# Performance work log

Measured on AMD Instinct MI355X. Metric: run time of the kernel, lower is better.

## Reference

```python
import jax, jax.numpy as jnp
import numpy as np
import math

B, I, O, SEG = 128, 2048, 2048, 10

def setup_inputs() -> dict:
    key = jax.random.key(0)
    k1, k2, k3, k4 = jax.random.split(key, 4)
    scale = 1.0 / math.sqrt(I)
    return {
        "x": jax.random.normal(k1, (B, I), dtype=jnp.float32),
        "context": jax.random.normal(k2, (O,), dtype=jnp.float32),
        "prev_activation": jax.random.normal(k3, (B, O), dtype=jnp.float32),
        "weight": jax.random.normal(k4, (O, I), dtype=jnp.float32) * scale,
        "bias": jnp.zeros((O,), dtype=jnp.float32),
        "astrocyte_activation": jnp.ones((O,), dtype=jnp.float32),
        "dendrite_segments": jax.random.normal(jax.random.fold_in(key, 7), (O, I, SEG), dtype=jnp.float32) * scale,
    }

def reference(x, context, prev_activation, weight, bias, astrocyte_activation, dendrite_segments):
    # Astrocyte gating of the linear weight: sigmoid(astro * context) -> [o]
    astro_mod = jax.nn.sigmoid(astrocyte_activation * context)
    # Dendritic branch: relu(einsum('bi,oij->boj')) summed over segments -> [b, o]
    dendritic_out = jnp.maximum(jnp.einsum('bi,oij->boj', x, dendrite_segments), 0.0).sum(axis=2)
    # Gated linear: F.linear(x, weight * astro_mod[:, None], bias) -> [b, o]
    out = x @ (weight * astro_mod[:, None]).T + bias
    # Note: torch's STDP/Hebbian weight mutations (synaptic_tag, protein_synthesis,
    # homeostatic scaling) occur AFTER 'out' is computed and do not affect the
    # returned tensor; they are pure parameter side effects, so omitted here.
    return out + dendritic_out
```

## Files before the change

### kernel.cpp

```cpp
#include <hip/hip_runtime.h>
#include <hip/hip_bf16.h>

#define B_ 128
#define I_ 2048
#define O_ 2048
#define SEG 10
#define BK 32
#define NST (I_ / BK)
#define XTILE 8192
#define DCH 1280
#define DLS 1408

typedef __attribute__((ext_vector_type(8))) short bf16x8;
typedef __attribute__((ext_vector_type(4))) float f32x4;

static __device__ __forceinline__ unsigned short f2bf(float f) {
    unsigned u = __float_as_uint(f);
    u += 0x7FFFu + ((u >> 16) & 1u);
    return (unsigned short)(u >> 16);
}

static __device__ __forceinline__ unsigned cvt2(float lo, float hi) {
    __hip_bfloat162 h = __float22bfloat162_rn(make_float2(lo, hi));
    return *reinterpret_cast<unsigned*>(&h);
}

#define GLDS16(SRC, DST) \
    __builtin_amdgcn_global_load_lds( \
        (const __attribute__((address_space(1))) unsigned*)(SRC), \
        (__attribute__((address_space(3))) unsigned*)(DST), 16, 0, 0)
#define GLDS4(SRC, DST) \
    __builtin_amdgcn_global_load_lds( \
        (const __attribute__((address_space(1))) unsigned*)(SRC), \
        (__attribute__((address_space(3))) unsigned*)(DST), 4, 0, 0)

#define WAITVM(N) asm volatile("s_waitcnt vmcnt(" #N ")" ::: "memory")
#define BARRIER() do { __builtin_amdgcn_sched_barrier(0); \
                       __builtin_amdgcn_s_barrier(); \
                       __builtin_amdgcn_sched_barrier(0); } while (0)

__global__ void xconv(const float* __restrict__ x, char* __restrict__ xb) {
    int idx = blockIdx.x * 256 + threadIdx.x;
    int row = idx >> 8;
    int c   = idx & 255;
    int k0  = c * 8;
    int tt  = k0 >> 5;
    int kl  = k0 & 31;

    const float* xp = x + (size_t)row * I_ + k0;
    float4 a = *reinterpret_cast<const float4*>(xp);
    float4 b = *reinterpret_cast<const float4*>(xp + 4);

    bf16x8 h;
    h[0] = (short)f2bf(a.x); h[1] = (short)f2bf(a.y);
    h[2] = (short)f2bf(a.z); h[3] = (short)f2bf(a.w);
    h[4] = (short)f2bf(b.x); h[5] = (short)f2bf(b.y);
    h[6] = (short)f2bf(b.z); h[7] = (short)f2bf(b.w);

    int sw = ((row >> 1) & 3) << 4;
    size_t off = (size_t)tt * XTILE + row * 64 + ((kl * 2) ^ sw);
    *reinterpret_cast<bf16x8*>(xb + off) = h;
}

__global__ __launch_bounds__(256, 2) void neuro_fused(
    const char*  __restrict__ xb,
    const float* __restrict__ ctx,
    const float* __restrict__ w,
    const float* __restrict__ bias,
    const float* __restrict__ astro,
    const float* __restrict__ D,
    float* __restrict__ out)
{
    __shared__ __align__(16) char xs[4][XTILE];
    __shared__ __align__(16) char dls[4][4][DLS];

    const int tid  = threadIdx.x;
    const int wv   = tid >> 6;
    const int lane = tid & 63;
    const bool isP = (wv < 2);
    const int o0   = blockIdx.x * 4;
    const int col  = lane & 15;
    const int g    = lane >> 4;

    const int p = wv;
    auto stage_x = [&](int t) {
        const char* src = xb + (size_t)t * XTILE + p * 4096 + lane * 16;
        char* dst = &xs[t & 3][p * 4096];
#pragma unroll
        for (int c = 0; c < 4; ++c)
            GLDS16(src + c * 1024, dst + c * 1024);
    };
    auto stage_d = [&](int t) {
#pragma unroll
        for (int q = 0; q < 2; ++q) {
            const int ol = 2 * p + q;
            const char* srcD = (const char*)D + (size_t)(o0 + ol) * (I_ * SEG * 4)
                             + (size_t)t * DCH;
            char* dst = &dls[ol][t & 3][0];
            GLDS16(srcD + lane * 16, dst);
            GLDS4(srcD + 1024 + lane * 4, dst + 1024);
            const char* srcW = (const char*)w + (size_t)(o0 + ol) * (I_ * 4) + t * (BK * 4);
            if (lane < 32) GLDS4(srcW + lane * 4, dst + DCH);
        }
    };

    const int c_ = wv - 2;
    f32x4 acc[2][8];
#pragma unroll
    for (int oo = 0; oo < 2; ++oo)
#pragma unroll
        for (int m = 0; m < 8; ++m) acc[oo][m] = (f32x4){0.f, 0.f, 0.f, 0.f};

    float am[2], bo[2];
    if (!isP) {
#pragma unroll
        for (int oo = 0; oo < 2; ++oo) {
            const int o = o0 + 2 * c_ + oo;
            float a = astro[o] * ctx[o];
            am[oo] = 1.0f / (1.0f + __expf(-a));
            bo[oo] = bias[o];
        }
    }

    const int fbase = (col < 10) ? col * 4 : DCH;
    const int fstr  = (col < 10) ? 40 : 4;
    const int sw    = ((col >> 1) & 3) << 4;

    auto compute = [&](int u) {
        const char* xbase = &xs[u & 3][0];
        bf16x8 af[8];
#pragma unroll
        for (int m = 0; m < 8; ++m)
            af[m] = *reinterpret_cast<const bf16x8*>(
                xbase + (m * 16 + col) * 64 + ((16 * g) ^ sw));
#pragma unroll
        for (int oo = 0; oo < 2; ++oo) {
            const char* fp = &dls[2 * c_ + oo][u & 3][0] + fbase + (8 * g) * fstr;
            float bv[8];
#pragma unroll
            for (int e = 0; e < 8; ++e)
                bv[e] = *reinterpret_cast<const float*>(fp + e * fstr);
            union { bf16x8 v; unsigned uu[4]; } bf;
#pragma unroll
            for (int e2 = 0; e2 < 4; ++e2)
                bf.uu[e2] = cvt2(bv[2 * e2], bv[2 * e2 + 1]);
#pragma unroll
            for (int m = 0; m < 8; ++m)
                acc[oo][m] = __builtin_amdgcn_mfma_f32_16x16x32_bf16(af[m], bf.v, acc[oo][m], 0, 0, 0);
        }
    };

    if (isP) {
        stage_x(0); stage_d(0);
        stage_x(1); stage_d(1);
        stage_x(2); stage_d(2);
        WAITVM(20);
    }

#pragma unroll 1
    for (int u = 0; u < NST; ++u) {
        BARRIER();
        if (isP) {
            if (u + 3 < NST) { stage_x(u + 3); stage_d(u + 3); }
            if (u <= NST - 4)      { WAITVM(20); }
            else if (u == NST - 3) { WAITVM(10); }
            else                   { WAITVM(0);  }
        } else {
            compute(u);
        }
    }

    if (!isP) {
#pragma unroll
        for (int oo = 0; oo < 2; ++oo) {
            const int o = o0 + 2 * c_ + oo;
#pragma unroll
            for (int m = 0; m < 8; ++m) {
#pragma unroll
                for (int r = 0; r < 4; ++r) {
                    float v = acc[oo][m][r];
                    float dend = (col < 10) ? fmaxf(v, 0.0f) : 0.0f;
#pragma unroll
                    for (int sh = 1; sh < 16; sh <<= 1)
                        dend += __shfl_xor(dend, sh, 64);
                    float lin = __shfl(v, (lane & 48) | 10, 64);
                    if (col == 0) {
                        int b = m * 16 + g * 4 + r;
                        out[(size_t)b * O_ + o] = dend + am[oo] * lin + bo[oo];
                    }
                }
            }
        }
    }
}

extern "C" void kernel_launch(void* const* d_in, const int* in_sizes, int n_in,
                              void* d_out, int out_size, void* d_ws, size_t ws_size,
                              hipStream_t stream) {
    const float* x     = (const float*)d_in[0];
    const float* ctx   = (const float*)d_in[1];
    const float* w     = (const float*)d_in[3];
    const float* bias  = (const float*)d_in[4];
    const float* astro = (const float*)d_in[5];
    const float* D     = (const float*)d_in[6];
    float* out = (float*)d_out;
    char* xb = (char*)d_ws;

    xconv<<<dim3(128), dim3(256), 0, stream>>>(x, xb);
    neuro_fused<<<dim3(512), dim3(256), 0, stream>>>(xb, ctx, w, bias, astro, D, out);
}
```

Before: 48.94 us.

## Load x fragments directly into registers with triple-buffered prefetch, drop LDS staging

Consumer waves now read the bf16 x tiles straight from global memory into three rotating register buffers, issuing loads three stages ahead. The x LDS buffer and its swizzle are removed, and producer waves only stage the dendrite and weight chunks, then exit early. The aim is to cut LDS traffic and producer load-issue work. In exchange, both consumer waves in each block fetch the full x tile, which doubles L2 reads of x. Picking a register buffer with a runtime u%3 also risks extra selects or scratch spills.

Result: slower. 102.2 us (+108.8%).

```diff
diff --git a/kernel.cpp b/kernel.cpp
--- a/kernel.cpp
+++ b/kernel.cpp
@@ -57,8 +57,7 @@
     h[4] = (short)f2bf(b.x); h[5] = (short)f2bf(b.y);
     h[6] = (short)f2bf(b.z); h[7] = (short)f2bf(b.w);
 
-    int sw = ((row >> 1) & 3) << 4;
-    size_t off = (size_t)tt * XTILE + row * 64 + ((kl * 2) ^ sw);
+    size_t off = (size_t)tt * XTILE + row * 64 + kl * 2;
     *reinterpret_cast<bf16x8*>(xb + off) = h;
 }
 
@@ -71,7 +70,6 @@
     const float* __restrict__ D,
     float* __restrict__ out)
 {
-    __shared__ __align__(16) char xs[4][XTILE];
     __shared__ __align__(16) char dls[4][4][DLS];
 
     const int tid  = threadIdx.x;
@@ -82,27 +80,35 @@
     const int col  = lane & 15;
     const int g    = lane >> 4;
 
-    const int p = wv;
-    auto stage_x = [&](int t) {
-        const char* src = xb + (size_t)t * XTILE + p * 4096 + lane * 16;
-        char* dst = &xs[t & 3][p * 4096];
-#pragma unroll
-        for (int c = 0; c < 4; ++c)
-            GLDS16(src + c * 1024, dst + c * 1024);
-    };
-    auto stage_d = [&](int t) {
-#pragma unroll
-        for (int q = 0; q < 2; ++q) {
-            const int ol = 2 * p + q;
-            const char* srcD = (const char*)D + (size_t)(o0 + ol) * (I_ * SEG * 4)
-                             + (size_t)t * DCH;
-            char* dst = &dls[ol][t & 3][0];
-            GLDS16(srcD + lane * 16, dst);
-            GLDS4(srcD + 1024 + lane * 4, dst + 1024);
-            const char* srcW = (const char*)w + (size_t)(o0 + ol) * (I_ * 4) + t * (BK * 4);
-            if (lane < 32) GLDS4(srcW + lane * 4, dst + DCH);
+    if (isP) {
+        const int p = wv;
+        auto stage_d = [&](int t) {
+#pragma unroll
+            for (int q = 0; q < 2; ++q) {
+                const int ol = 2 * p + q;
+                const char* srcD = (const char*)D + (size_t)(o0 + ol) * (I_ * SEG * 4)
+                                 + (size_t)t * DCH;
+                char* dst = &dls[ol][t & 3][0];
+                GLDS16(srcD + lane * 16, dst);
+                GLDS4(srcD + 1024 + lane * 4, dst + 1024);
+                const char* srcW = (const char*)w + (size_t)(o0 + ol) * (I_ * 4) + t * (BK * 4);
+                if (lane < 32) GLDS4(srcW + lane * 4, dst + DCH);
+            }
+        };
+
+        stage_d(0); stage_d(1); stage_d(2);
+        WAITVM(12);
+
+#pragma unroll 1
+        for (int u = 0; u < NST; ++u) {
+            BARRIER();
+            if (u + 3 < NST) stage_d(u + 3);
+            if (u <= NST - 4)      { WAITVM(12); }
+            else if (u == NST - 3) { WAITVM(6);  }
+            else                   { WAITVM(0);  }
         }
-    };
+        return;
+    }
 
     const int c_ = wv - 2;
     f32x4 acc[2][8];
@@ -112,27 +118,27 @@
         for (int m = 0; m < 8; ++m) acc[oo][m] = (f32x4){0.f, 0.f, 0.f, 0.f};
 
     float am[2], bo[2];
-    if (!isP) {
-#pragma unroll
-        for (int oo = 0; oo < 2; ++oo) {
-            const int o = o0 + 2 * c_ + oo;
-            float a = astro[o] * ctx[o];
-            am[oo] = 1.0f / (1.0f + __expf(-a));
-            bo[oo] = bias[o];
-        }
+#pragma unroll
+    for (int oo = 0; oo < 2; ++oo) {
+        const int o = o0 + 2 * c_ + oo;
+        float a = astro[o] * ctx[o];
+        am[oo] = 1.0f / (1.0f + __expf(-a));
+        bo[oo] = bias[o];
     }
 
     const int fbase = (col < 10) ? col * 4 : DCH;
     const int fstr  = (col < 10) ? 40 : 4;
-    const int sw    = ((col >> 1) & 3) << 4;
-
-    auto compute = [&](int u) {
-        const char* xbase = &xs[u & 3][0];
-        bf16x8 af[8];
+
+    const char* asrc = xb + col * 64 + g * 16;
+
+    auto issueA = [&](int t, bf16x8 (&dst)[8]) {
+        const char* src = asrc + (size_t)t * XTILE;
 #pragma unroll
         for (int m = 0; m < 8; ++m)
-            af[m] = *reinterpret_cast<const bf16x8*>(
-                xbase + (m * 16 + col) * 64 + ((16 * g) ^ sw));
+            dst[m] = *reinterpret_cast<const bf16x8*>(src + m * 1024);
+    };
+
+    auto compute = [&](int u, bf16x8 (&af)[8]) {
 #pragma unroll
         for (int oo = 0; oo < 2; ++oo) {
             const char* fp = &dls[2 * c_ + oo][u & 3][0] + fbase + (8 * g) * fstr;
@@ -150,44 +156,36 @@
         }
     };
 
-    if (isP) {
-        stage_x(0); stage_d(0);
-        stage_x(1); stage_d(1);
-        stage_x(2); stage_d(2);
-        WAITVM(20);
-    }
+    bf16x8 af0[8], af1[8], af2[8];
+    issueA(0, af0); issueA(1, af1); issueA(2, af2);
 
 #pragma unroll 1
     for (int u = 0; u < NST; ++u) {
         BARRIER();
-        if (isP) {
-            if (u + 3 < NST) { stage_x(u + 3); stage_d(u + 3); }
-            if (u <= NST - 4)      { WAITVM(20); }
-            else if (u == NST - 3) { WAITVM(10); }
-            else                   { WAITVM(0);  }
-        } else {
-            compute(u);
-        }
-    }
-
-    if (!isP) {
-#pragma unroll
-        for (int oo = 0; oo < 2; ++oo) {
-            const int o = o0 + 2 * c_ + oo;
-#pragma unroll
-            for (int m = 0; m < 8; ++m) {
-#pragma unroll
-                for (int r = 0; r < 4; ++r) {
-                    float v = acc[oo][m][r];
-                    float dend = (col < 10) ? fmaxf(v, 0.0f) : 0.0f;
-#pragma unroll
-                    for (int sh = 1; sh < 16; sh <<= 1)
-                        dend += __shfl_xor(dend, sh, 64);
-                    float lin = __shfl(v, (lane & 48) | 10, 64);
-                    if (col == 0) {
-                        int b = m * 16 + g * 4 + r;
-                        out[(size_t)b * O_ + o] = dend + am[oo] * lin + bo[oo];
-                    }
+        if (u <= NST - 3)      { WAITVM(16); }
+        else if (u == NST - 2) { WAITVM(8);  }
+        else                   { WAITVM(0);  }
+        bf16x8 (&af)[8] = (u % 3 == 0) ? af0 : (u % 3 == 1) ? af1 : af2;
+        compute(u, af);
+        if (u + 3 < NST) issueA(u + 3, af);
+    }
+
+#pragma unroll
+    for (int oo = 0; oo < 2; ++oo) {
+        const int o = o0 + 2 * c_ + oo;
+#pragma unroll
+        for (int m = 0; m < 8; ++m) {
+#pragma unroll
+            for (int r = 0; r < 4; ++r) {
+                float v = acc[oo][m][r];
+                float dend = (col < 10) ? fmaxf(v, 0.0f) : 0.0f;
+#pragma unroll
+                for (int sh = 1; sh < 16; sh <<= 1)
+                    dend += __shfl_xor(dend, sh, 64);
+                float lin = __shfl(v, (lane & 48) | 10, 64);
+                if (col == 0) {
+                    int b = m * 16 + g * 4 + r;
+                    out[(size_t)b * O_ + o] = dend + am[oo] * lin + bo[oo];
                 }
             }
         }
```
